# Kernel tuning notes

Hardware: AMD Instinct MI355X
Metric: run time of the kernel (lower is better)

The kernel has to match this reference:

```python
import jax, jax.numpy as jnp
import numpy as np
import math

B, L, HID, NH = 4, 4096, 1024, 8
DH = HID // NH
THETA = 10000.0


def _rope_tables(seq_len, dh):
    half = dh // 2
    inv_freq = 1.0 / (THETA ** (jnp.arange(half, dtype=jnp.float32) / half))
    freqs = jnp.arange(seq_len, dtype=jnp.float32)[:, None] * inv_freq[None, :]  # [L, half]
    return jnp.cos(freqs), jnp.sin(freqs)


def _apply_rope(x, cos, sin):
    # x: [B,H,L,D], D even
    half = x.shape[-1] // 2
    x1, x2 = x[..., :half], x[..., half:2 * half]
    c = cos[None, None]
    s = sin[None, None]
    return jnp.concatenate([x1 * c - x2 * s, x1 * s + x2 * c], axis=-1)


def setup_inputs() -> dict:
    key = jax.random.key(0)
    ks = jax.random.split(key, 9)
    def xav(k, sh):
        lim = math.sqrt(6.0 / (sh[0] + sh[1]))
        return jax.random.uniform(k, sh, jnp.float32, -lim, lim)
    return {
        "x": jax.random.normal(ks[0], (B, L, HID), jnp.float32),
        "norm_w": jnp.ones((HID,), jnp.float32),
        "Wq": xav(ks[1], (HID, HID)),
        "Wk": xav(ks[2], (HID, HID)),
        "Wv": xav(ks[3], (HID, HID)),
        "Wbeta": xav(ks[4], (NH, HID)),
        "bbeta": jnp.full((NH,), 2.0, jnp.float32),  # retention-favoring init
        "Wig": xav(ks[5], (NH, HID)),
        "big": jnp.zeros((NH,), jnp.float32),
        "Wog": xav(ks[6], (NH, HID)),
        "bog": jnp.zeros((NH,), jnp.float32),
        "Wout": xav(ks[7], (HID, HID)),
        "bout": jnp.zeros((HID,), jnp.float32),
    }


def reference(x, norm_w, Wq, Wk, Wv, Wbeta, bbeta, Wig, big, Wog, bog, Wout, bout):
    Bq, Lq, _ = x.shape
    # RMSNorm (no mean subtraction)
    h = x * jax.lax.rsqrt(jnp.mean(x * x, axis=-1, keepdims=True) + 1e-6) * norm_w
    # q/k/v projections (torch Linear: h @ W.T), split heads -> [B,H,L,Dh]
    def heads(W):
        return jnp.einsum('bld,ed->ble', h, W).reshape(Bq, Lq, NH, DH).transpose(0, 2, 1, 3)
    q, k, v = heads(Wq), heads(Wk), heads(Wv)
    cos, sin = _rope_tables(Lq, DH)
    q = _apply_rope(q, cos, sin)
    k = _apply_rope(k, cos, sin)
    # token-conditional gates -> [B,H,L]
    def gate(W, b):
        return jax.nn.sigmoid(jnp.einsum('bld,hd->blh', h, W) + b).transpose(0, 2, 1)
    beta, ig, og = gate(Wbeta, bbeta), gate(Wig, big), gate(Wog, bog)
    scale = 1.0 / math.sqrt(DH)
    # time-major for the sequential delta-rule scan
    qT = q.transpose(2, 0, 1, 3)  # [L,B,H,D]
    kT = k.transpose(2, 0, 1, 3)
    vT = v.transpose(2, 0, 1, 3)
    fT = beta.transpose(2, 0, 1)  # [L,B,H]
    gT = ig.transpose(2, 0, 1)
    oT = og.transpose(2, 0, 1)
    M0 = jnp.zeros((Bq, NH, DH, DH), x.dtype)
    def step(M, inp):
        q_t, k_t, v_t, f_t, g_t, o_t = inp
        M = M * f_t[..., None, None] + (g_t[..., None, None] * scale) * (k_t[..., :, None] * v_t[..., None, :])
        y_t = jnp.einsum('bhd,bhde->bhe', q_t, M) * o_t[..., None]
        return M, y_t
    _, yT = jax.lax.scan(step, M0, (qT, kT, vT, fT, gT, oT))  # yT: [L,B,H,D]
    y = yT.transpose(1, 0, 2, 3).reshape(Bq, Lq, HID)  # b l (h d)
    return jnp.einsum('bld,ed->ble', y, Wout) + bout
```

## Files before the change

kernel.cpp:

```cpp
#include <hip/hip_runtime.h>
#include <hip/hip_bf16.h>

#define BQ 4
#define LQ 4096
#define HID 1024
#define NHEAD 8
#define DHEAD 128
#define MROWS (BQ * LQ)
#define CCH 64
#define NCH (LQ / CCH)
#define GNT 16

typedef __bf16 bf16x8 __attribute__((ext_vector_type(8)));
typedef float f32x4 __attribute__((ext_vector_type(4)));

__device__ __forceinline__ float bf2f(unsigned short u) {
    return __uint_as_float(((unsigned int)u) << 16);
}
__device__ __forceinline__ unsigned short f2us(float f) {
    __hip_bfloat16 b = __float2bfloat16(f);
    return *reinterpret_cast<unsigned short*>(&b);
}
__device__ __forceinline__ float loadAny(const void* p, size_t i, bool isf) {
    return isf ? ((const float*)p)[i] : bf2f(((const unsigned short*)p)[i]);
}

__global__ void detect_kernel(const void* x, int* flag) {
    const unsigned short* u = (const unsigned short*)x;
    int t = threadIdx.x;
    int cnt = 0;
#pragma unroll
    for (int s = 0; s < 64; ++s) {
        unsigned short v = u[2 * (t * 64 + s)];
        int e = (v >> 7) & 0xFF;
        cnt += (e >= 0x8A || (e != 0 && e <= 0x6E)) ? 1 : 0;
    }
#pragma unroll
    for (int m = 1; m < 64; m <<= 1) cnt += __shfl_xor(cnt, m);
    if (t == 0) *flag = (cnt > 1024) ? 1 : 0;
}

__global__ __launch_bounds__(256) void cvt_w4_kernel(
    const void* Wq, const void* Wk, const void* Wv, const void* Wout,
    unsigned short* dq, unsigned short* dk, unsigned short* dv, unsigned short* dout,
    float* __restrict__ cosT, float* __restrict__ sinT,
    const int* flagp) {
    if (blockIdx.y == 4) {
        int idx = blockIdx.x * 256 + threadIdx.x;
        int l = idx >> 6, i = idx & 63;
        float invf = powf(10000.0f, -(float)i * (1.0f / 64.0f));
        float fr = (float)l * invf;
        cosT[idx] = cosf(fr);
        sinT[idx] = sinf(fr);
        return;
    }
    const bool isf = (*flagp != 0);
    const void* s;
    unsigned short* d;
    switch (blockIdx.y) {
        case 0: s = Wq; d = dq; break;
        case 1: s = Wk; d = dk; break;
        case 2: s = Wv; d = dv; break;
        default: s = Wout; d = dout; break;
    }
    size_t i = ((size_t)blockIdx.x * 256 + threadIdx.x) * 4;
#pragma unroll
    for (int r = 0; r < 4; ++r) d[i + r] = f2us(loadAny(s, i + r, isf));
}

__global__ __launch_bounds__(256) void cvt_small_kernel(
    const void* Wbeta, const void* Wig, const void* Wog,
    const void* bbeta, const void* big, const void* bog, const void* bout,
    unsigned short* dWb, unsigned short* dWi, unsigned short* dWo,
    float* dbb, float* dbi, float* dbo, float* dbout,
    const int* flagp) {
    const bool isf = (*flagp != 0);
    int gid = blockIdx.x * 256 + threadIdx.x;
    if (gid < 24576) {
        int seg = gid >> 13, off = gid & 8191;
        const void* s = (seg == 0) ? Wbeta : (seg == 1) ? Wig : Wog;
        unsigned short* d = (seg == 0) ? dWb : (seg == 1) ? dWi : dWo;
        d[off] = f2us(loadAny(s, off, isf));
    } else {
        int j = gid - 24576;
        if (j < 8) dbb[j] = loadAny(bbeta, j, isf);
        else if (j < 16) dbi[j - 8] = loadAny(big, j - 8, isf);
        else if (j < 24) dbo[j - 16] = loadAny(bog, j - 16, isf);
        else if (j < 24 + 1024) dbout[j - 24] = loadAny(bout, j - 24, isf);
    }
}

__global__ __launch_bounds__(256) void rmsnorm_gates_kernel(
    const void* __restrict__ xin, const void* __restrict__ win,
    __hip_bfloat16* __restrict__ h, const int* __restrict__ flagp,
    const __hip_bfloat16* __restrict__ Wbeta, const float* __restrict__ bbeta,
    const __hip_bfloat16* __restrict__ Wig, const float* __restrict__ big,
    const __hip_bfloat16* __restrict__ Wog, const float* __restrict__ bog,
    float* __restrict__ fT, float* __restrict__ gT, float* __restrict__ oT) {
    const bool isf = (*flagp != 0);
    const int row = blockIdx.x;
    const int tid = threadIdx.x;
    const int lane = tid & 63, wave = tid >> 6;
    const int b = row >> 12, l = row & (LQ - 1);
    const size_t base = (size_t)row * HID;
    float x0, x1, x2, x3;
    if (isf) {
        float4 u = ((const float4*)((const float*)xin + base))[tid];
        x0 = u.x; x1 = u.y; x2 = u.z; x3 = u.w;
    } else {
        ushort4 u = ((const ushort4*)((const unsigned short*)xin + base))[tid];
        x0 = bf2f(u.x); x1 = bf2f(u.y); x2 = bf2f(u.z); x3 = bf2f(u.w);
    }
    float ss = x0 * x0 + x1 * x1 + x2 * x2 + x3 * x3;
#pragma unroll
    for (int m = 1; m < 64; m <<= 1) ss += __shfl_xor(ss, m);
    __shared__ float wsum[4];
    if (lane == 0) wsum[wave] = ss;
    __syncthreads();
    float tot = wsum[0] + wsum[1] + wsum[2] + wsum[3];
    float inv = rsqrtf(tot * (1.0f / HID) + 1e-6f);
    float w0, w1, w2, w3;
    if (isf) {
        float4 u = ((const float4*)win)[tid];
        w0 = u.x; w1 = u.y; w2 = u.z; w3 = u.w;
    } else {
        ushort4 u = ((const ushort4*)win)[tid];
        w0 = bf2f(u.x); w1 = bf2f(u.y); w2 = bf2f(u.z); w3 = bf2f(u.w);
    }
    float h0 = x0 * inv * w0, h1 = x1 * inv * w1, h2 = x2 * inv * w2, h3 = x3 * inv * w3;
    __hip_bfloat16* ho = h + base + tid * 4;
    ho[0] = __float2bfloat16(h0);
    ho[1] = __float2bfloat16(h1);
    ho[2] = __float2bfloat16(h2);
    ho[3] = __float2bfloat16(h3);
    float p[24];
#pragma unroll
    for (int g = 0; g < 24; ++g) {
        const __hip_bfloat16* wr = (g < 8) ? (Wbeta + g * HID)
                                 : (g < 16) ? (Wig + (g - 8) * HID)
                                            : (Wog + (g - 16) * HID);
        const unsigned short* wp = (const unsigned short*)wr + tid * 4;
        ushort4 wu = *(const ushort4*)wp;
        p[g] = h0 * bf2f(wu.x) + h1 * bf2f(wu.y) + h2 * bf2f(wu.z) + h3 * bf2f(wu.w);
    }
#pragma unroll
    for (int m = 1; m < 64; m <<= 1) {
#pragma unroll
        for (int g = 0; g < 24; ++g) p[g] += __shfl_xor(p[g], m);
    }
    __shared__ float part[4][24];
    if (lane == 0) {
#pragma unroll
        for (int g = 0; g < 24; ++g) part[wave][g] = p[g];
    }
    __syncthreads();
    if (tid < 24) {
        int g = tid;
        float s = part[0][g] + part[1][g] + part[2][g] + part[3][g];
        float bb = (g < 8) ? bbeta[g] : (g < 16) ? big[g - 8] : bog[g - 16];
        s += bb;
        s = 1.0f / (1.0f + expf(-s));
        int hh = (g < 8) ? g : (g < 16) ? g - 8 : g - 16;
        float* dst = (g < 8) ? fT : (g < 16) ? gT : oT;
        dst[((size_t)(b * NHEAD + hh)) * LQ + l] = s;
    }
}

__device__ __forceinline__ void g256_stage_half(const unsigned short* __restrict__ src,
                                                unsigned short* lds, int tid) {
#pragma unroll
    for (int l = 0; l < 2; ++l) {
        int L = l * 512 + tid;
        int r = L >> 3, g = L & 7;
        int gs = g ^ (r & 7);
        __builtin_amdgcn_global_load_lds(
            (const __attribute__((address_space(1))) void*)(src + (size_t)r * HID + gs * 8),
            (__attribute__((address_space(3))) void*)(lds + L * 8), 16, 0, 0);
    }
}

#define G256_SEAL() __builtin_amdgcn_sched_barrier(0)
#define G256_BARRIER()            \
    do {                          \
        G256_SEAL();              \
        __builtin_amdgcn_s_barrier(); \
        G256_SEAL();              \
    } while (0)
#define G256_LGKM0()                                        \
    do {                                                    \
        asm volatile("s_waitcnt lgkmcnt(0)" ::: "memory");  \
        G256_SEAL();                                        \
    } while (0)

__device__ __forceinline__ void g256_read_A(const unsigned short* Ac, int mq,
                                            int wr, int lm, int lq, bf16x8 (&bA)[4][2]) {
#pragma unroll
    for (int i = 0; i < 4; ++i) {
        const int row = mq * 128 + wr * 64 + i * 16 + lm;
#pragma unroll
        for (int kk = 0; kk < 2; ++kk) {
            const int gsw = (kk * 4 + lq) ^ (lm & 7);
            bA[i][kk] = *(const bf16x8*)(const void*)(Ac + row * 64 + gsw * 8);
        }
    }
}
__device__ __forceinline__ void g256_read_B(const unsigned short* Bc, int nq,
                                            int wc, int lm, int lq, bf16x8 (&bB)[2][2]) {
#pragma unroll
    for (int j = 0; j < 2; ++j) {
        const int row = nq * 128 + wc * 32 + j * 16 + lm;
#pragma unroll
        for (int kk = 0; kk < 2; ++kk) {
            const int gsw = (kk * 4 + lq) ^ (lm & 7);
            bB[j][kk] = *(const bf16x8*)(const void*)(Bc + row * 64 + gsw * 8);
        }
    }
}
__device__ __forceinline__ void g256_mfma(int mq, int nq, const bf16x8 (&bA)[4][2],
                                          const bf16x8 (&bB)[2][2], f32x4 (&acc)[8][4]) {
    __builtin_amdgcn_s_setprio(1);
#pragma unroll
    for (int i = 0; i < 4; ++i)
#pragma unroll
        for (int j = 0; j < 2; ++j)
#pragma unroll
            for (int kk = 0; kk < 2; ++kk)
                acc[mq * 4 + i][nq * 2 + j] = __builtin_amdgcn_mfma_f32_16x16x32_bf16(
                    bA[i][kk], bB[j][kk], acc[mq * 4 + i][nq * 2 + j], 0, 0, 0);
    __builtin_amdgcn_s_setprio(0);
}

__device__ __forceinline__ void g256_core(const unsigned short* __restrict__ A,
                                          const unsigned short* __restrict__ W,
                                          unsigned short* As, unsigned short* Bs,
                                          int m0, int tid, f32x4 (&acc)[8][4]) {
    const int lane = tid & 63, wid = tid >> 6;
    const int wr = wid >> 2, wc = wid & 3;
    const int lm = lane & 15, lq = lane >> 4;
    g256_stage_half(A + (size_t)m0 * HID, As, tid);
    g256_stage_half(W, Bs, tid);
    g256_stage_half(W + (size_t)128 * HID, Bs + 8192, tid);
    g256_stage_half(A + (size_t)(m0 + 128) * HID, As + 8192, tid);
    G256_SEAL();
    asm volatile("s_waitcnt vmcnt(0)" ::: "memory");
    G256_BARRIER();
    for (int t = 0; t < GNT; ++t) {
        unsigned short* Ac = As + (t & 1) * 16384;
        unsigned short* Bc = Bs + (t & 1) * 16384;
        unsigned short* An = As + ((t & 1) ^ 1) * 16384;
        unsigned short* Bn = Bs + ((t & 1) ^ 1) * 16384;
        const int kn = (t + 1) * 64;
        const bool pf = (t + 1 < GNT);
        bf16x8 bA[4][2], bB0[2][2], bB1[2][2];
        g256_read_A(Ac, 0, wr, lm, lq, bA);
        g256_read_B(Bc, 0, wc, lm, lq, bB0);
        if (pf) {
            g256_stage_half(A + (size_t)m0 * HID + kn, An, tid);
            g256_stage_half(W + kn, Bn, tid);
        }
        G256_BARRIER();
        G256_LGKM0();
        g256_mfma(0, 0, bA, bB0, acc);
        G256_BARRIER();
        g256_read_B(Bc, 1, wc, lm, lq, bB1);
        if (pf) g256_stage_half(W + (size_t)128 * HID + kn, Bn + 8192, tid);
        G256_BARRIER();
        G256_LGKM0();
        g256_mfma(0, 1, bA, bB1, acc);
        G256_BARRIER();
        g256_read_A(Ac, 1, wr, lm, lq, bA);
        if (pf) g256_stage_half(A + (size_t)(m0 + 128) * HID + kn, An + 8192, tid);
        G256_BARRIER();
        G256_LGKM0();
        g256_mfma(1, 0, bA, bB0, acc);
        G256_BARRIER();
        g256_mfma(1, 1, bA, bB1, acc);
        G256_SEAL();
        if (pf) asm volatile("s_waitcnt vmcnt(0)" ::: "memory");
        G256_BARRIER();
    }
}

__global__ __launch_bounds__(512) void gemm_qkv(const __hip_bfloat16* __restrict__ A,
                                                const unsigned short* __restrict__ Wqc,
                                                const unsigned short* __restrict__ Wkc,
                                                const unsigned short* __restrict__ Wvc,
                                                unsigned short* __restrict__ qb,
                                                unsigned short* __restrict__ kb,
                                                unsigned short* __restrict__ vb) {
    __shared__ __align__(16) unsigned short As[2 * 16384];
    __shared__ __align__(16) unsigned short Bs[2 * 16384];
    const int nblk = blockIdx.y;
    const int sel = nblk >> 2;
    const int nl0 = (nblk & 3) * 256;
    const unsigned short* W = (sel == 0 ? Wqc : sel == 1 ? Wkc : Wvc) + (size_t)nl0 * HID;
    unsigned short* C = (sel == 0) ? qb : (sel == 1) ? kb : vb;
    const int tid = threadIdx.x;
    const int lane = tid & 63, wid = tid >> 6;
    const int wr = wid >> 2, wc = wid & 3;
    const int lm = lane & 15, lq = lane >> 4;
    const int m0 = blockIdx.x * 256;
    f32x4 acc[8][4] = {};
    g256_core((const unsigned short*)A, W, As, Bs, m0, tid, acc);
#pragma unroll
    for (int mq = 0; mq < 2; ++mq)
#pragma unroll
        for (int i = 0; i < 4; ++i)
#pragma unroll
            for (int nq = 0; nq < 2; ++nq)
#pragma unroll
                for (int j = 0; j < 2; ++j) {
                    const int col = nl0 + nq * 128 + wc * 32 + j * 16 + lm;
#pragma unroll
                    for (int r = 0; r < 4; ++r) {
                        const int rowg = m0 + mq * 128 + wr * 64 + i * 16 + lq * 4 + r;
                        C[(size_t)rowg * HID + col] = f2us(acc[mq * 4 + i][nq * 2 + j][r]);
                    }
                }
}

__global__ __launch_bounds__(512) void gemm_bt(const __hip_bfloat16* __restrict__ A,
                                               const __hip_bfloat16* __restrict__ W,
                                               const float* __restrict__ bias,
                                               void* __restrict__ C,
                                               const int* __restrict__ flagp) {
    __shared__ __align__(16) unsigned short As[2 * 16384];
    __shared__ __align__(16) unsigned short Bs[2 * 16384];
    const bool f32out = (*flagp != 0);
    const int tid = threadIdx.x;
    const int lane = tid & 63, wid = tid >> 6;
    const int wr = wid >> 2, wc = wid & 3;
    const int lm = lane & 15, lq = lane >> 4;
    const int m0 = blockIdx.x * 256;
    const int nl0 = blockIdx.y * 256;
    f32x4 acc[8][4] = {};
    g256_core((const unsigned short*)A, (const unsigned short*)W + (size_t)nl0 * HID,
              As, Bs, m0, tid, acc);
#pragma unroll
    for (int mq = 0; mq < 2; ++mq)
#pragma unroll
        for (int i = 0; i < 4; ++i)
#pragma unroll
            for (int nq = 0; nq < 2; ++nq)
#pragma unroll
                for (int j = 0; j < 2; ++j) {
                    const int col = nl0 + nq * 128 + wc * 32 + j * 16 + lm;
                    const float bv = bias[col];
#pragma unroll
                    for (int r = 0; r < 4; ++r) {
                        const int rowg = m0 + mq * 128 + wr * 64 + i * 16 + lq * 4 + r;
                        const size_t idx = (size_t)rowg * HID + col;
                        const float val = acc[mq * 4 + i][nq * 2 + j][r] + bv;
                        if (f32out) ((float*)C)[idx] = val;
                        else ((__hip_bfloat16*)C)[idx] = __float2bfloat16(val);
                    }
                }
}

__global__ __launch_bounds__(256) void intra_kernel(
    unsigned short* __restrict__ qg, const unsigned short* __restrict__ kg,
    const unsigned short* __restrict__ vg,
    const float* __restrict__ fT, const float* __restrict__ gT, const float* __restrict__ oT,
    const float* __restrict__ cosT, const float* __restrict__ sinT,
    __hip_bfloat16* __restrict__ yb,
    unsigned short* __restrict__ ktg, float* __restrict__ cdecG) {
    const int chunk = blockIdx.x;
    const int bh = blockIdx.y;
    const int b = bh >> 3, hh = bh & 7;
    const int t0 = chunk * CCH;
    const int tid = threadIdx.x;
    const int lane = tid & 63, wave = tid >> 6;
    const int lm = lane & 15, lq = lane >> 4;
    __shared__ unsigned short Kr[64 * 136];
    __shared__ unsigned short Vt[128 * 72];
    __shared__ unsigned short Sp[64 * 72];
    __shared__ float Lp[64], aS[64], osh[64], w2s[64], qscs[64];

    if (tid < 64) {
        float f = fT[(size_t)bh * LQ + t0 + tid];
        float g = gT[(size_t)bh * LQ + t0 + tid];
        osh[tid] = oT[(size_t)bh * LQ + t0 + tid];
        float lf = __logf(f);
#pragma unroll
        for (int off = 1; off < 64; off <<= 1) {
            float v = __shfl_up(lf, off);
            if (lane >= off) lf += v;
        }
        float tot = __shfl(lf, 63);
        Lp[tid] = lf;
        aS[tid] = g * 0.08838834764831845f;
        w2s[tid] = __expf(tot - lf) * (g * 0.08838834764831845f);
        qscs[tid] = __expf(lf);
        if (tid == 63) cdecG[bh * NCH + chunk] = __expf(lf);
    }
    __syncthreads();

    bf16x8 af[4];
    {
        const int jr = 16 * wave + lm;
        const int gt = t0 + jr;
        const size_t qbase = ((size_t)(b * LQ + gt)) * HID + hh * DHEAD;
        uint4 qraw[4];
#pragma unroll
        for (int ks = 0; ks < 4; ++ks)
            qraw[ks] = *(const uint4*)(qg + qbase + ks * 32 + lq * 8);
        const unsigned short* q0 = (const unsigned short*)&qraw[0];
        const unsigned short* q1 = (const unsigned short*)&qraw[1];
        const unsigned short* q2 = (const unsigned short*)&qraw[2];
        const unsigned short* q3 = (const unsigned short*)&qraw[3];
        const float sc = qscs[jr];
        __align__(16) unsigned short fr[4][8];
        __align__(16) unsigned short qo[4][8];
#pragma unroll
        for (int u = 0; u < 8; ++u) {
            int i = lq * 8 + u;
            int i2 = 32 + lq * 8 + u;
            float c0 = cosT[gt * 64 + i], s0 = sinT[gt * 64 + i];
            float c1 = cosT[gt * 64 + i2], s1 = sinT[gt * 64 + i2];
            float a = bf2f(q0[u]), bq = bf2f(q2[u]);
            float rc = a * c0 - bq * s0, rs = a * s0 + bq * c0;
            fr[0][u] = f2us(rc); fr[2][u] = f2us(rs);
            qo[0][u] = f2us(rc * sc); qo[2][u] = f2us(rs * sc);
            float a1 = bf2f(q1[u]), bq1 = bf2f(q3[u]);
            float rc1 = a1 * c1 - bq1 * s1, rs1 = a1 * s1 + bq1 * c1;
            fr[1][u] = f2us(rc1); fr[3][u] = f2us(rs1);
            qo[1][u] = f2us(rc1 * sc); qo[3][u] = f2us(rs1 * sc);
        }
#pragma unroll
        for (int ks = 0; ks < 4; ++ks) {
            af[ks] = *(const bf16x8*)fr[ks];
            *(uint4*)(qg + qbase + ks * 32 + lq * 8) = *(const uint4*)qo[ks];
        }
    }
#pragma unroll
    for (int r = 0; r < 16; ++r) {
        int pid = r * 256 + tid;
        int t = pid >> 6, i = pid & 63;
        int gt = t0 + t;
        size_t gidx = ((size_t)(b * LQ + gt)) * HID + hh * DHEAD + i;
        float c = cosT[gt * 64 + i], s = sinT[gt * 64 + i];
        float k1 = bf2f(kg[gidx]), k2 = bf2f(kg[gidx + 64]);
        Kr[t * 136 + i] = f2us(k1 * c - k2 * s);
        Kr[t * 136 + i + 64] = f2us(k1 * s + k2 * c);
    }
#pragma unroll
    for (int r = 0; r < 32; ++r) {
        int lin = r * 256 + tid;
        int sI = lin >> 7, e = lin & 127;
        float val = bf2f(vg[((size_t)(b * LQ + t0 + sI)) * HID + hh * DHEAD + e]);
        Vt[e * 72 + sI] = f2us(val);
    }
    __syncthreads();

    f32x4 sacc[4] = {};
#pragma unroll
    for (int ks = 0; ks < 4; ++ks) {
#pragma unroll
        for (int nt = 0; nt < 4; ++nt) {
            bf16x8 bf = *(const bf16x8*)(const void*)(Kr + (nt * 16 + lm) * 136 + ks * 32 + lq * 8);
            sacc[nt] = __builtin_amdgcn_mfma_f32_16x16x32_bf16(af[ks], bf, sacc[nt], 0, 0, 0);
        }
    }
#pragma unroll
    for (int nt = 0; nt < 4; ++nt) {
#pragma unroll
        for (int r = 0; r < 4; ++r) {
            int j = 16 * wave + lq * 4 + r;
            int s = nt * 16 + lm;
            float v = 0.0f;
            if (j >= s) v = sacc[nt][r] * __expf(Lp[j] - Lp[s]) * aS[s];
            Sp[j * 72 + s] = f2us(v);
        }
    }
    {
        unsigned short* krec = ktg + ((size_t)(bh * NCH + chunk)) * 8192;
#pragma unroll
        for (int r = 0; r < 2; ++r) {
            int lin16 = r * 256 + tid;
            int ks = lin16 >> 8;
            int d = (lin16 & 255) >> 1;
            int cc0 = (lin16 & 1) * 16;
            __align__(16) unsigned short out[16];
#pragma unroll
            for (int u = 0; u < 16; ++u) {
                int s = ks * 32 + cc0 + u;
                out[u] = f2us(w2s[s] * bf2f(Kr[s * 136 + d]));
            }
            uint4* dst = (uint4*)(krec + (size_t)lin16 * 16);
            dst[0] = *(const uint4*)(out);
            dst[1] = *(const uint4*)(out + 8);
        }
    }
    __syncthreads();

    f32x4 ya[8] = {};
#pragma unroll
    for (int ks = 0; ks < 2; ++ks) {
        bf16x8 afs = *(const bf16x8*)(const void*)(Sp + (16 * wave + lm) * 72 + ks * 32 + lq * 8);
#pragma unroll
        for (int nt = 0; nt < 8; ++nt) {
            bf16x8 bf = *(const bf16x8*)(const void*)(Vt + (nt * 16 + lm) * 72 + ks * 32 + lq * 8);
            ya[nt] = __builtin_amdgcn_mfma_f32_16x16x32_bf16(afs, bf, ya[nt], 0, 0, 0);
        }
    }
#pragma unroll
    for (int nt = 0; nt < 8; ++nt) {
#pragma unroll
        for (int r = 0; r < 4; ++r) {
            int j = 16 * wave + lq * 4 + r;
            int e = nt * 16 + lm;
            size_t row = (size_t)(b * LQ + t0 + j);
            yb[row * HID + hh * DHEAD + e] = __float2bfloat16(osh[j] * ya[nt][r]);
        }
    }
}

__global__ __launch_bounds__(256) void inter_kernel(
    const unsigned short* __restrict__ qs,
    const unsigned short* __restrict__ ktg,
    const unsigned short* __restrict__ vg,
    const float* __restrict__ oT, const float* __restrict__ cdecG,
    unsigned short* __restrict__ yb) {
    const int bh = blockIdx.x;
    const int esplit = blockIdx.y;
    const int e0 = esplit * 16;
    const int b = bh >> 3, hh = bh & 7;
    const int tid = threadIdx.x;
    const int lane = tid & 63, wave = tid >> 6;
    const int lm = lane & 15, lq = lane >> 4;
    __shared__ __align__(16) unsigned short Qsl[2][8192];
    __shared__ __align__(16) unsigned short Ktl[2][8192];
    __shared__ __align__(16) unsigned short Vtl[2][1024];
    __shared__ __align__(16) float Ml[2][16 * 132];

    for (int i = tid; i < 16 * 132; i += 256) Ml[0][i] = 0.0f;

    const int jrow = tid >> 2;
    const int qcol = (tid & 3) * 8;
    {
        const unsigned short* qrow =
            qs + ((size_t)(b * LQ + jrow)) * HID + hh * DHEAD + qcol;
#pragma unroll
        for (int ks = 0; ks < 4; ++ks)
            __builtin_amdgcn_global_load_lds(
                (const __attribute__((address_space(1))) void*)(qrow + ks * 32),
                (__attribute__((address_space(3))) void*)(&Qsl[0][ks * 2048 + tid * 8]),
                16, 0, 0);
        const unsigned short* kbase = ktg + ((size_t)(bh * NCH)) * 8192 + tid * 8;
#pragma unroll
        for (int i = 0; i < 4; ++i)
            __builtin_amdgcn_global_load_lds(
                (const __attribute__((address_space(1))) void*)(kbase + i * 2048),
                (__attribute__((address_space(3))) void*)(&Ktl[0][i * 2048 + tid * 8]),
                16, 0, 0);
#pragma unroll
        for (int r = 0; r < 4; ++r) {
            int lin = r * 256 + tid;
            int s = lin >> 4, e = lin & 15;
            float val = bf2f(vg[((size_t)(b * LQ + s)) * HID + hh * DHEAD + e0 + e]);
            Vtl[0][(s >> 5) * 512 + e * 32 + (s & 31)] = f2us(val);
        }
    }

    for (int c = 0; c < NCH; ++c) {
        const int cur = c & 1, nxt = cur ^ 1;
        const int t0 = c * CCH;
        __syncthreads();
        if (c + 1 < NCH) {
            const int t0n = t0 + CCH;
            const unsigned short* qrow =
                qs + ((size_t)(b * LQ + t0n + jrow)) * HID + hh * DHEAD + qcol;
#pragma unroll
            for (int ks = 0; ks < 4; ++ks)
                __builtin_amdgcn_global_load_lds(
                    (const __attribute__((address_space(1))) void*)(qrow + ks * 32),
                    (__attribute__((address_space(3))) void*)(&Qsl[nxt][ks * 2048 + tid * 8]),
                    16, 0, 0);
            const unsigned short* kbase = ktg + ((size_t)(bh * NCH + c + 1)) * 8192 + tid * 8;
#pragma unroll
            for (int i = 0; i < 4; ++i)
                __builtin_amdgcn_global_load_lds(
                    (const __attribute__((address_space(1))) void*)(kbase + i * 2048),
                    (__attribute__((address_space(3))) void*)(&Ktl[nxt][i * 2048 + tid * 8]),
                    16, 0, 0);
        }
        size_t yidx[4];
        unsigned short prevy[4];
        float osv[4];
#pragma unroll
        for (int r = 0; r < 4; ++r) {
            int j = 16 * wave + lq * 4 + r;
            yidx[r] = ((size_t)(b * LQ + t0 + j)) * HID + hh * DHEAD + e0 + lm;
            prevy[r] = yb[yidx[r]];
            osv[r] = oT[(size_t)bh * LQ + t0 + j];
        }
        const float cd = cdecG[bh * NCH + c];
        f32x4 uacc[2] = {};
#pragma unroll
        for (int ks = 0; ks < 2; ++ks) {
            bf16x8 bfv = *(const bf16x8*)(const void*)(&Vtl[cur][ks * 512 + lm * 32 + lq * 8]);
#pragma unroll
            for (int mt = 0; mt < 2; ++mt) {
                bf16x8 af = *(const bf16x8*)(const void*)(
                    &Ktl[cur][ks * 4096 + (32 * wave + 16 * mt + lm) * 32 + lq * 8]);
                uacc[mt] = __builtin_amdgcn_mfma_f32_16x16x32_bf16(af, bfv, uacc[mt], 0, 0, 0);
            }
        }
        f32x4 yacc = {};
#pragma unroll
        for (int ks = 0; ks < 4; ++ks) {
            bf16x8 af = *(const bf16x8*)(const void*)(
                &Qsl[cur][ks * 2048 + (16 * wave + lm) * 32 + lq * 8]);
            float4 m0 = *(const float4*)(const void*)(&Ml[cur][lm * 132 + ks * 32 + lq * 8]);
            float4 m1 = *(const float4*)(const void*)(&Ml[cur][lm * 132 + ks * 32 + lq * 8 + 4]);
            __align__(16) unsigned short tmp[8];
            tmp[0] = f2us(m0.x); tmp[1] = f2us(m0.y); tmp[2] = f2us(m0.z); tmp[3] = f2us(m0.w);
            tmp[4] = f2us(m1.x); tmp[5] = f2us(m1.y); tmp[6] = f2us(m1.z); tmp[7] = f2us(m1.w);
            bf16x8 bfm = *(const bf16x8*)tmp;
            yacc = __builtin_amdgcn_mfma_f32_16x16x32_bf16(af, bfm, yacc, 0, 0, 0);
        }
#pragma unroll
        for (int r = 0; r < 4; ++r)
            yb[yidx[r]] = f2us(bf2f(prevy[r]) + osv[r] * yacc[r]);
        if (c + 1 < NCH) {
            const int t0n = t0 + CCH;
#pragma unroll
            for (int r = 0; r < 4; ++r) {
                int lin = r * 256 + tid;
                int s = lin >> 4, e = lin & 15;
                float val = bf2f(vg[((size_t)(b * LQ + t0n + s)) * HID + hh * DHEAD + e0 + e]);
                Vtl[nxt][(s >> 5) * 512 + e * 32 + (s & 31)] = f2us(val);
            }
        }
#pragma unroll
        for (int mt = 0; mt < 2; ++mt)
#pragma unroll
            for (int r = 0; r < 4; ++r) {
                int d = 32 * wave + 16 * mt + lq * 4 + r;
                Ml[nxt][lm * 132 + d] = cd * Ml[cur][lm * 132 + d] + uacc[mt][r];
            }
    }
}

extern "C" void kernel_launch(void* const* d_in, const int* in_sizes, int n_in,
                              void* d_out, int out_size, void* d_ws, size_t ws_size,
                              hipStream_t stream) {
    const void* x      = d_in[0];
    const void* norm_w = d_in[1];
    const void* Wq     = d_in[2];
    const void* Wk     = d_in[3];
    const void* Wv     = d_in[4];
    const void* Wbeta  = d_in[5];
    const void* bbeta  = d_in[6];
    const void* Wig    = d_in[7];
    const void* big    = d_in[8];
    const void* Wog    = d_in[9];
    const void* bog    = d_in[10];
    const void* Wout   = d_in[11];
    const void* bout   = d_in[12];

    char* ws = (char*)d_ws;
    const size_t KB = 1024, MB = 1024 * 1024;
    int*   flag    = (int*)(ws + 0);
    float* bbeta_c = (float*)(ws + 1 * KB);
    float* big_c   = (float*)(ws + 1 * KB + 32);
    float* bog_c   = (float*)(ws + 1 * KB + 64);
    float* bout_c  = (float*)(ws + 4 * KB);
    float* cdecG   = (float*)(ws + 16 * KB);
    unsigned short* Wbeta_c = (unsigned short*)(ws + 64 * KB);
    unsigned short* Wig_c   = (unsigned short*)(ws + 96 * KB);
    unsigned short* Wog_c   = (unsigned short*)(ws + 128 * KB);
    float* fT   = (float*)(ws + 1 * MB);
    float* gT   = (float*)(ws + 1 * MB + 512 * KB);
    float* oT   = (float*)(ws + 2 * MB);
    float* cosT = (float*)(ws + 2 * MB + 512 * KB);
    float* sinT = (float*)(ws + 3 * MB + 512 * KB);
    unsigned short* Wq_c   = (unsigned short*)(ws + 5 * MB);
    unsigned short* Wk_c   = (unsigned short*)(ws + 7 * MB);
    unsigned short* Wv_c   = (unsigned short*)(ws + 9 * MB);
    unsigned short* Wout_c = (unsigned short*)(ws + 11 * MB);
    __hip_bfloat16* h  = (__hip_bfloat16*)(ws + 16 * MB);
    unsigned short* ktg = (unsigned short*)(ws + 16 * MB);
    unsigned short* qb = (unsigned short*)(ws + 48 * MB);
    unsigned short* kb = (unsigned short*)(ws + 80 * MB);
    unsigned short* vb = (unsigned short*)(ws + 112 * MB);
    __hip_bfloat16* yb = (__hip_bfloat16*)(ws + 144 * MB);

    detect_kernel<<<1, 64, 0, stream>>>(x, flag);
    cvt_w4_kernel<<<dim3(1024, 5), 256, 0, stream>>>(Wq, Wk, Wv, Wout,
                                                     Wq_c, Wk_c, Wv_c, Wout_c,
                                                     cosT, sinT, flag);
    cvt_small_kernel<<<101, 256, 0, stream>>>(Wbeta, Wig, Wog, bbeta, big, bog, bout,
                                              Wbeta_c, Wig_c, Wog_c,
                                              bbeta_c, big_c, bog_c, bout_c, flag);
    rmsnorm_gates_kernel<<<MROWS, 256, 0, stream>>>(
        x, norm_w, h, flag,
        (const __hip_bfloat16*)Wbeta_c, bbeta_c,
        (const __hip_bfloat16*)Wig_c, big_c,
        (const __hip_bfloat16*)Wog_c, bog_c, fT, gT, oT);

    gemm_qkv<<<dim3(MROWS / 256, 12), 512, 0, stream>>>(h, Wq_c, Wk_c, Wv_c, qb, kb, vb);

    intra_kernel<<<dim3(NCH, 32), 256, 0, stream>>>(qb, kb, vb, fT, gT, oT, cosT, sinT,
                                                    (__hip_bfloat16*)yb, ktg, cdecG);
    inter_kernel<<<dim3(32, 8), 256, 0, stream>>>(qb, ktg, vb, oT, cdecG,
                                                  (unsigned short*)yb);

    gemm_bt<<<dim3(MROWS / 256, HID / 256), 512, 0, stream>>>(
        (const __hip_bfloat16*)yb, (const __hip_bfloat16*)Wout_c, bout_c, d_out, flag);
}
```

Before: 507.5 us.

## Move gate projections into QKV GEMM as extra padded N-block

Removes the 24-way gate dot products and cross-lane reductions from the RMSNorm kernel. The gate weights go into a zero-padded 256-row bf16 matrix, which gemm_qkv handles as a 13th N-block, applying bias and sigmoid in its epilogue. The RMSNorm kernel now only writes h, using one vectorized store per thread. The cost is a GEMM tile that is mostly padding (24 of 256 columns are useful), plus an extra grid column and scattered fp32 gate stores.

```diff
diff --git a/kernel.cpp b/kernel.cpp
--- a/kernel.cpp
+++ b/kernel.cpp
@@ -71,7 +71,7 @@
 __global__ __launch_bounds__(256) void cvt_small_kernel(
     const void* Wbeta, const void* Wig, const void* Wog,
     const void* bbeta, const void* big, const void* bog, const void* bout,
-    unsigned short* dWb, unsigned short* dWi, unsigned short* dWo,
+    unsigned short* __restrict__ Wg_pad,
     float* dbb, float* dbi, float* dbo, float* dbout,
     const int* flagp) {
     const bool isf = (*flagp != 0);
@@ -79,29 +79,29 @@
     if (gid < 24576) {
         int seg = gid >> 13, off = gid & 8191;
         const void* s = (seg == 0) ? Wbeta : (seg == 1) ? Wig : Wog;
-        unsigned short* d = (seg == 0) ? dWb : (seg == 1) ? dWi : dWo;
-        d[off] = f2us(loadAny(s, off, isf));
-    } else {
+        Wg_pad[gid] = f2us(loadAny(s, off, isf));
+    } else if (gid < 25624) {
         int j = gid - 24576;
         if (j < 8) dbb[j] = loadAny(bbeta, j, isf);
         else if (j < 16) dbi[j - 8] = loadAny(big, j - 8, isf);
         else if (j < 24) dbo[j - 16] = loadAny(bog, j - 16, isf);
         else if (j < 24 + 1024) dbout[j - 24] = loadAny(bout, j - 24, isf);
-    }
-}
-
-__global__ __launch_bounds__(256) void rmsnorm_gates_kernel(
+    } else {
+        int z = gid - 25624;
+        if (z < 29696) {
+            uint4 zz = make_uint4(0, 0, 0, 0);
+            *(uint4*)(Wg_pad + 24576 + (size_t)z * 8) = zz;
+        }
+    }
+}
+
+__global__ __launch_bounds__(256) void rmsnorm_kernel(
     const void* __restrict__ xin, const void* __restrict__ win,
-    __hip_bfloat16* __restrict__ h, const int* __restrict__ flagp,
-    const __hip_bfloat16* __restrict__ Wbeta, const float* __restrict__ bbeta,
-    const __hip_bfloat16* __restrict__ Wig, const float* __restrict__ big,
-    const __hip_bfloat16* __restrict__ Wog, const float* __restrict__ bog,
-    float* __restrict__ fT, float* __restrict__ gT, float* __restrict__ oT) {
+    __hip_bfloat16* __restrict__ h, const int* __restrict__ flagp) {
     const bool isf = (*flagp != 0);
     const int row = blockIdx.x;
     const int tid = threadIdx.x;
     const int lane = tid & 63, wave = tid >> 6;
-    const int b = row >> 12, l = row & (LQ - 1);
     const size_t base = (size_t)row * HID;
     float x0, x1, x2, x3;
     if (isf) {
@@ -127,43 +127,12 @@
         ushort4 u = ((const ushort4*)win)[tid];
         w0 = bf2f(u.x); w1 = bf2f(u.y); w2 = bf2f(u.z); w3 = bf2f(u.w);
     }
-    float h0 = x0 * inv * w0, h1 = x1 * inv * w1, h2 = x2 * inv * w2, h3 = x3 * inv * w3;
-    __hip_bfloat16* ho = h + base + tid * 4;
-    ho[0] = __float2bfloat16(h0);
-    ho[1] = __float2bfloat16(h1);
-    ho[2] = __float2bfloat16(h2);
-    ho[3] = __float2bfloat16(h3);
-    float p[24];
-#pragma unroll
-    for (int g = 0; g < 24; ++g) {
-        const __hip_bfloat16* wr = (g < 8) ? (Wbeta + g * HID)
-                                 : (g < 16) ? (Wig + (g - 8) * HID)
-                                            : (Wog + (g - 16) * HID);
-        const unsigned short* wp = (const unsigned short*)wr + tid * 4;
-        ushort4 wu = *(const ushort4*)wp;
-        p[g] = h0 * bf2f(wu.x) + h1 * bf2f(wu.y) + h2 * bf2f(wu.z) + h3 * bf2f(wu.w);
-    }
-#pragma unroll
-    for (int m = 1; m < 64; m <<= 1) {
-#pragma unroll
-        for (int g = 0; g < 24; ++g) p[g] += __shfl_xor(p[g], m);
-    }
-    __shared__ float part[4][24];
-    if (lane == 0) {
-#pragma unroll
-        for (int g = 0; g < 24; ++g) part[wave][g] = p[g];
-    }
-    __syncthreads();
-    if (tid < 24) {
-        int g = tid;
-        float s = part[0][g] + part[1][g] + part[2][g] + part[3][g];
-        float bb = (g < 8) ? bbeta[g] : (g < 16) ? big[g - 8] : bog[g - 16];
-        s += bb;
-        s = 1.0f / (1.0f + expf(-s));
-        int hh = (g < 8) ? g : (g < 16) ? g - 8 : g - 16;
-        float* dst = (g < 8) ? fT : (g < 16) ? gT : oT;
-        dst[((size_t)(b * NHEAD + hh)) * LQ + l] = s;
-    }
+    ushort4 ho4;
+    ho4.x = f2us(x0 * inv * w0);
+    ho4.y = f2us(x1 * inv * w1);
+    ho4.z = f2us(x2 * inv * w2);
+    ho4.w = f2us(x3 * inv * w3);
+    *(ushort4*)((unsigned short*)h + base + tid * 4) = ho4;
 }
 
 __device__ __forceinline__ void g256_stage_half(const unsigned short* __restrict__ src,
@@ -285,16 +254,26 @@
                                                 const unsigned short* __restrict__ Wqc,
                                                 const unsigned short* __restrict__ Wkc,
                                                 const unsigned short* __restrict__ Wvc,
+                                                const unsigned short* __restrict__ Wg_pad,
                                                 unsigned short* __restrict__ qb,
                                                 unsigned short* __restrict__ kb,
-                                                unsigned short* __restrict__ vb) {
+                                                unsigned short* __restrict__ vb,
+                                                const float* __restrict__ bbeta,
+                                                const float* __restrict__ big,
+                                                const float* __restrict__ bog,
+                                                float* __restrict__ fT,
+                                                float* __restrict__ gT,
+                                                float* __restrict__ oT) {
     __shared__ __align__(16) unsigned short As[2 * 16384];
     __shared__ __align__(16) unsigned short Bs[2 * 16384];
     const int nblk = blockIdx.y;
     const int sel = nblk >> 2;
     const int nl0 = (nblk & 3) * 256;
-    const unsigned short* W = (sel == 0 ? Wqc : sel == 1 ? Wkc : Wvc) + (size_t)nl0 * HID;
-    unsigned short* C = (sel == 0) ? qb : (sel == 1) ? kb : vb;
+    const unsigned short* W =
+        (sel == 0) ? Wqc + (size_t)nl0 * HID
+      : (sel == 1) ? Wkc + (size_t)nl0 * HID
+      : (sel == 2) ? Wvc + (size_t)nl0 * HID
+                   : Wg_pad;
     const int tid = threadIdx.x;
     const int lane = tid & 63, wid = tid >> 6;
     const int wr = wid >> 2, wc = wid & 3;
@@ -302,21 +281,48 @@
     const int m0 = blockIdx.x * 256;
     f32x4 acc[8][4] = {};
     g256_core((const unsigned short*)A, W, As, Bs, m0, tid, acc);
-#pragma unroll
-    for (int mq = 0; mq < 2; ++mq)
-#pragma unroll
-        for (int i = 0; i < 4; ++i)
-#pragma unroll
-            for (int nq = 0; nq < 2; ++nq)
-#pragma unroll
-                for (int j = 0; j < 2; ++j) {
-                    const int col = nl0 + nq * 128 + wc * 32 + j * 16 + lm;
-#pragma unroll
-                    for (int r = 0; r < 4; ++r) {
-                        const int rowg = m0 + mq * 128 + wr * 64 + i * 16 + lq * 4 + r;
-                        C[(size_t)rowg * HID + col] = f2us(acc[mq * 4 + i][nq * 2 + j][r]);
+    if (sel < 3) {
+        unsigned short* C = (sel == 0) ? qb : (sel == 1) ? kb : vb;
+#pragma unroll
+        for (int mq = 0; mq < 2; ++mq)
+#pragma unroll
+            for (int i = 0; i < 4; ++i)
+#pragma unroll
+                for (int nq = 0; nq < 2; ++nq)
+#pragma unroll
+                    for (int j = 0; j < 2; ++j) {
+                        const int col = nl0 + nq * 128 + wc * 32 + j * 16 + lm;
+#pragma unroll
+                        for (int r = 0; r < 4; ++r) {
+                            const int rowg = m0 + mq * 128 + wr * 64 + i * 16 + lq * 4 + r;
+                            C[(size_t)rowg * HID + col] = f2us(acc[mq * 4 + i][nq * 2 + j][r]);
+                        }
                     }
-                }
+    } else {
+#pragma unroll
+        for (int j = 0; j < 2; ++j) {
+            const int col = wc * 32 + j * 16 + lm;
+            if (col < 24) {
+                const float bb = (col < 8) ? bbeta[col]
+                               : (col < 16) ? big[col - 8]
+                                            : bog[col - 16];
+                const int hh = col & 7;
+                float* dst = (col < 8) ? fT : (col < 16) ? gT : oT;
+#pragma unroll
+                for (int mq = 0; mq < 2; ++mq)
+#pragma unroll
+                    for (int i = 0; i < 4; ++i)
+#pragma unroll
+                        for (int r = 0; r < 4; ++r) {
+                            const int rowg = m0 + mq * 128 + wr * 64 + i * 16 + lq * 4 + r;
+                            const int b = rowg >> 12, l = rowg & (LQ - 1);
+                            float s = acc[mq * 4 + i][j][r] + bb;
+                            s = 1.0f / (1.0f + expf(-s));
+                            dst[((size_t)(b * NHEAD + hh)) * LQ + l] = s;
+                        }
+            }
+        }
+    }
 }
 
 __global__ __launch_bounds__(512) void gemm_bt(const __hip_bfloat16* __restrict__ A,
@@ -667,9 +673,6 @@
     float* bog_c   = (float*)(ws + 1 * KB + 64);
     float* bout_c  = (float*)(ws + 4 * KB);
     float* cdecG   = (float*)(ws + 16 * KB);
-    unsigned short* Wbeta_c = (unsigned short*)(ws + 64 * KB);
-    unsigned short* Wig_c   = (unsigned short*)(ws + 96 * KB);
-    unsigned short* Wog_c   = (unsigned short*)(ws + 128 * KB);
     float* fT   = (float*)(ws + 1 * MB);
     float* gT   = (float*)(ws + 1 * MB + 512 * KB);
     float* oT   = (float*)(ws + 2 * MB);
@@ -679,6 +682,7 @@
     unsigned short* Wk_c   = (unsigned short*)(ws + 7 * MB);
     unsigned short* Wv_c   = (unsigned short*)(ws + 9 * MB);
     unsigned short* Wout_c = (unsigned short*)(ws + 11 * MB);
+    unsigned short* Wg_pad = (unsigned short*)(ws + 13 * MB);
     __hip_bfloat16* h  = (__hip_bfloat16*)(ws + 16 * MB);
     unsigned short* ktg = (unsigned short*)(ws + 16 * MB);
     unsigned short* qb = (unsigned short*)(ws + 48 * MB);
@@ -690,16 +694,14 @@
     cvt_w4_kernel<<<dim3(1024, 5), 256, 0, stream>>>(Wq, Wk, Wv, Wout,
                                                      Wq_c, Wk_c, Wv_c, Wout_c,
                                                      cosT, sinT, flag);
-    cvt_small_kernel<<<101, 256, 0, stream>>>(Wbeta, Wig, Wog, bbeta, big, bog, bout,
-                                              Wbeta_c, Wig_c, Wog_c,
+    cvt_small_kernel<<<217, 256, 0, stream>>>(Wbeta, Wig, Wog, bbeta, big, bog, bout,
+                                              Wg_pad,
                                               bbeta_c, big_c, bog_c, bout_c, flag);
-    rmsnorm_gates_kernel<<<MROWS, 256, 0, stream>>>(
-        x, norm_w, h, flag,
-        (const __hip_bfloat16*)Wbeta_c, bbeta_c,
-        (const __hip_bfloat16*)Wig_c, big_c,
-        (const __hip_bfloat16*)Wog_c, bog_c, fT, gT, oT);
-
-    gemm_qkv<<<dim3(MROWS / 256, 12), 512, 0, stream>>>(h, Wq_c, Wk_c, Wv_c, qb, kb, vb);
+    rmsnorm_kernel<<<MROWS, 256, 0, stream>>>(x, norm_w, h, flag);
+
+    gemm_qkv<<<dim3(MROWS / 256, 13), 512, 0, stream>>>(
+        h, Wq_c, Wk_c, Wv_c, Wg_pad, qb, kb, vb,
+        bbeta_c, big_c, bog_c, fT, gT, oT);
 
     intra_kernel<<<dim3(NCH, 32), 256, 0, stream>>>(qb, kb, vb, fT, gT, oT, cosT, sinT,
                                                     (__hip_bfloat16*)yb, ktg, cdecG);
```

Result: faster. 447.5 us (-11.8%).
